# Performance work log

Measured on AMD Instinct MI355X. Metric: run time of the kernel, lower is better.

## Reference

```python
import jax, jax.numpy as jnp
import numpy as np

GAMMA = 1.0

def setup_inputs() -> dict:
    key = jax.random.key(0)
    kx, ky = jax.random.split(key)
    x = jax.random.normal(kx, (8192, 64), dtype=jnp.float32)
    y = jax.random.normal(ky, (8192, 64), dtype=jnp.float32)
    return {"x": x, "y": y}

def reference(x, y):
    # RBF kernel K[b,a] = exp(-gamma * ||x_b - y_a||^2)
    # broadcast intermediate of the naive formulation (same math).
    x_sq = jnp.sum(x * x, axis=-1)                    # (B,)
    y_sq = jnp.sum(y * y, axis=-1)                    # (A,)
    xy = jnp.einsum('bd,ad->ba', x, y)                # (B, A) GEMM
    dist_sq = x_sq[:, None] + y_sq[None, :] - 2.0 * xy
    dist_sq = jnp.maximum(dist_sq, 0.0)               # numeric floor
    return jnp.exp(-GAMMA * dist_sq)
```

## Files before the change

kernel.cpp:

```cpp
#include <hip/hip_runtime.h>

#define D    64
#define NROW 8192

typedef _Float16 f16x8 __attribute__((ext_vector_type(8)));
typedef float    f32x4 __attribute__((ext_vector_type(4)));

__global__ __launch_bounds__(256, 3) void rbf_fused(const float* __restrict__ x,
                                                    const float* __restrict__ y,
                                                    float* __restrict__ out) {
    __shared__ __align__(16) char YH[16384];
    __shared__ __align__(16) char YL[16384];
    __shared__ float Ysq0[128];
    __shared__ float Ysq1[128];

    const int t    = threadIdx.x;
    const int col0 = blockIdx.x * 128;
    const int row0 = blockIdx.y * 128;

    {
        const int r    = t & 127;
        const int half = t >> 7;
        const int swz  = (r & 7) << 4;
        const float* yp = y + (size_t)(col0 + r) * D + half * 32;
        float ssq = 0.f;
#pragma unroll
        for (int it = 0; it < 4; ++it) {
            float4 b0 = *reinterpret_cast<const float4*>(yp + it * 8);
            float4 b1 = *reinterpret_cast<const float4*>(yp + it * 8 + 4);
            float v[8] = {b0.x, b0.y, b0.z, b0.w, b1.x, b1.y, b1.z, b1.w};
            f16x8 h, l;
#pragma unroll
            for (int j = 0; j < 8; ++j) {
                _Float16 hh = (_Float16)v[j];
                h[j] = hh;
                l[j] = (_Float16)(v[j] - (float)hh);
                ssq  = fmaf(v[j], v[j], ssq);
            }
            const int off = r * 128 + ((half * 64 + it * 16) ^ swz);
            *reinterpret_cast<f16x8*>(YH + off) = h;
            *reinterpret_cast<f16x8*>(YL + off) = l;
        }
        if (half == 0) Ysq0[r] = ssq; else Ysq1[r] = ssq;
    }

    const int lane = t & 63;
    const int w    = t >> 6;
    const int l15  = lane & 15;
    const int lg   = lane >> 4;

    f16x8 xh[2][2], xl[2][2];
    float xsq[2];
#pragma unroll
    for (int i = 0; i < 2; ++i) {
        const float* xp = x + (size_t)(row0 + w * 32 + i * 16 + l15) * D + lg * 8;
        float s = 0.f;
#pragma unroll
        for (int kh = 0; kh < 2; ++kh) {
            float4 a0 = *reinterpret_cast<const float4*>(xp + kh * 32);
            float4 a1 = *reinterpret_cast<const float4*>(xp + kh * 32 + 4);
            float v[8] = {a0.x, a0.y, a0.z, a0.w, a1.x, a1.y, a1.z, a1.w};
#pragma unroll
            for (int j = 0; j < 8; ++j) {
                _Float16 hh = (_Float16)v[j];
                xh[i][kh][j] = hh;
                xl[i][kh][j] = (_Float16)(v[j] - (float)hh);
                s = fmaf(v[j], v[j], s);
            }
        }
        s += __shfl_xor(s, 16);
        s += __shfl_xor(s, 32);
        xsq[i] = s;
    }
    __syncthreads();

    f32x4 acc[2][8];
#pragma unroll
    for (int i = 0; i < 2; ++i)
#pragma unroll
        for (int nt = 0; nt < 8; ++nt) acc[i][nt] = (f32x4){0.f, 0.f, 0.f, 0.f};

    const int swzA = (l15 & 7) << 4;
#pragma unroll
    for (int kh = 0; kh < 2; ++kh) {
        const int dsw = (kh * 64 + lg * 16) ^ swzA;
#pragma unroll
        for (int nt = 0; nt < 8; ++nt) {
            const int aoff = (nt * 16 + l15) * 128 + dsw;
            f16x8 yh = *reinterpret_cast<const f16x8*>(YH + aoff);
            f16x8 yl = *reinterpret_cast<const f16x8*>(YL + aoff);
            acc[0][nt] = __builtin_amdgcn_mfma_f32_16x16x32_f16(yh, xh[0][kh], acc[0][nt], 0, 0, 0);
            acc[1][nt] = __builtin_amdgcn_mfma_f32_16x16x32_f16(yh, xh[1][kh], acc[1][nt], 0, 0, 0);
            acc[0][nt] = __builtin_amdgcn_mfma_f32_16x16x32_f16(yl, xh[0][kh], acc[0][nt], 0, 0, 0);
            acc[1][nt] = __builtin_amdgcn_mfma_f32_16x16x32_f16(yl, xh[1][kh], acc[1][nt], 0, 0, 0);
            acc[0][nt] = __builtin_amdgcn_mfma_f32_16x16x32_f16(yh, xl[0][kh], acc[0][nt], 0, 0, 0);
            acc[1][nt] = __builtin_amdgcn_mfma_f32_16x16x32_f16(yh, xl[1][kh], acc[1][nt], 0, 0, 0);
        }
    }

#pragma unroll
    for (int nt = 0; nt < 8; ++nt) {
        const int c = nt * 16 + lg * 4;
        float4 p0 = *reinterpret_cast<const float4*>(&Ysq0[c]);
        float4 p1 = *reinterpret_cast<const float4*>(&Ysq1[c]);
        float ysqv[4] = {p0.x + p1.x, p0.y + p1.y, p0.z + p1.z, p0.w + p1.w};
#pragma unroll
        for (int i = 0; i < 2; ++i) {
            const int rowg = row0 + w * 32 + i * 16 + l15;
            float e[4];
#pragma unroll
            for (int r = 0; r < 4; ++r) {
                float d2 = fmaf(-2.f, acc[i][nt][r], xsq[i] + ysqv[r]);
                d2 = fmaxf(d2, 0.f);
                e[r] = __expf(-d2);
            }
            *reinterpret_cast<float4*>(out + (size_t)rowg * NROW + col0 + c) =
                make_float4(e[0], e[1], e[2], e[3]);
        }
    }
}

extern "C" void kernel_launch(void* const* d_in, const int* in_sizes, int n_in,
                              void* d_out, int out_size, void* d_ws, size_t ws_size,
                              hipStream_t stream) {
    const float* x = (const float*)d_in[0];
    const float* y = (const float*)d_in[1];
    float* out = (float*)d_out;
    (void)d_ws; (void)ws_size;

    rbf_fused<<<dim3(NROW / 128, NROW / 128), 256, 0, stream>>>(x, y, out);
}
```

Measured before the change: 67.22 us.

## Precompute fp16 hi/lo splits and row norms in a prepass kernel

Adds a prepass kernel that converts x and y once into fp16 hi/lo planes plus squared norms in the workspace. The main kernel then loads these directly, so the per-block float-to-half splitting and norm reductions, which were repeated by every block in a row or column of the grid, go away. In exchange it adds an extra kernel launch and workspace traffic, and it falls back to the fused kernel when the workspace is too small. The main kernel is output-write bound (256MB), so the gain may be small.

Result: slower. 72.79 us (+8.3%).

```diff
diff --git a/kernel.cpp b/kernel.cpp
--- a/kernel.cpp
+++ b/kernel.cpp
@@ -5,6 +5,128 @@
 
 typedef _Float16 f16x8 __attribute__((ext_vector_type(8)));
 typedef float    f32x4 __attribute__((ext_vector_type(4)));
+
+__global__ __launch_bounds__(256) void rbf_split(const float* __restrict__ x,
+                                                 const float* __restrict__ y,
+                                                 _Float16* __restrict__ hi,
+                                                 _Float16* __restrict__ lo,
+                                                 float* __restrict__ sq) {
+    const int tid    = blockIdx.x * 256 + threadIdx.x;
+    const int rowAll = tid >> 3;
+    const int dp     = (tid & 7) * 8;
+    const float* src = (rowAll < NROW) ? (x + (size_t)rowAll * D)
+                                       : (y + (size_t)(rowAll - NROW) * D);
+    float4 a0 = *reinterpret_cast<const float4*>(src + dp);
+    float4 a1 = *reinterpret_cast<const float4*>(src + dp + 4);
+    float v[8] = {a0.x, a0.y, a0.z, a0.w, a1.x, a1.y, a1.z, a1.w};
+    f16x8 h, l;
+    float s = 0.f;
+#pragma unroll
+    for (int j = 0; j < 8; ++j) {
+        _Float16 hh = (_Float16)v[j];
+        h[j] = hh;
+        l[j] = (_Float16)(v[j] - (float)hh);
+        s = fmaf(v[j], v[j], s);
+    }
+    *reinterpret_cast<f16x8*>(hi + (size_t)rowAll * D + dp) = h;
+    *reinterpret_cast<f16x8*>(lo + (size_t)rowAll * D + dp) = l;
+    s += __shfl_xor(s, 1);
+    s += __shfl_xor(s, 2);
+    s += __shfl_xor(s, 4);
+    if ((tid & 7) == 0) sq[rowAll] = s;
+}
+
+__global__ __launch_bounds__(256, 3) void rbf_main2(const _Float16* __restrict__ hi,
+                                                    const _Float16* __restrict__ lo,
+                                                    const float* __restrict__ sq,
+                                                    float* __restrict__ out) {
+    __shared__ __align__(16) char YH[16384];
+    __shared__ __align__(16) char YL[16384];
+
+    const int t    = threadIdx.x;
+    const int col0 = blockIdx.x * 128;
+    const int row0 = blockIdx.y * 128;
+
+    {
+        const int r   = t & 127;
+        const int hb  = t >> 7;
+        const int swz = (r & 7) << 4;
+        const _Float16* gh = hi + (size_t)(NROW + col0 + r) * D;
+        const _Float16* gl = lo + (size_t)(NROW + col0 + r) * D;
+#pragma unroll
+        for (int it = 0; it < 4; ++it) {
+            const int c16 = hb * 4 + it;
+            const int off = r * 128 + ((c16 * 16) ^ swz);
+            *reinterpret_cast<f16x8*>(YH + off) =
+                *reinterpret_cast<const f16x8*>(gh + c16 * 8);
+            *reinterpret_cast<f16x8*>(YL + off) =
+                *reinterpret_cast<const f16x8*>(gl + c16 * 8);
+        }
+    }
+
+    const int lane = t & 63;
+    const int w    = t >> 6;
+    const int l15  = lane & 15;
+    const int lg   = lane >> 4;
+
+    f16x8 xh[2][2], xl[2][2];
+    float xsq[2];
+#pragma unroll
+    for (int i = 0; i < 2; ++i) {
+        const size_t xoff = (size_t)(row0 + w * 32 + i * 16 + l15) * D + lg * 8;
+#pragma unroll
+        for (int kh = 0; kh < 2; ++kh) {
+            xh[i][kh] = *reinterpret_cast<const f16x8*>(hi + xoff + kh * 32);
+            xl[i][kh] = *reinterpret_cast<const f16x8*>(lo + xoff + kh * 32);
+        }
+        xsq[i] = sq[row0 + w * 32 + i * 16 + l15];
+    }
+    __syncthreads();
+
+    f32x4 acc[2][8];
+#pragma unroll
+    for (int i = 0; i < 2; ++i)
+#pragma unroll
+        for (int nt = 0; nt < 8; ++nt) acc[i][nt] = (f32x4){0.f, 0.f, 0.f, 0.f};
+
+    const int swzA = (l15 & 7) << 4;
+#pragma unroll
+    for (int kh = 0; kh < 2; ++kh) {
+        const int dsw = (kh * 64 + lg * 16) ^ swzA;
+#pragma unroll
+        for (int nt = 0; nt < 8; ++nt) {
+            const int aoff = (nt * 16 + l15) * 128 + dsw;
+            f16x8 ah = *reinterpret_cast<const f16x8*>(YH + aoff);
+            f16x8 al = *reinterpret_cast<const f16x8*>(YL + aoff);
+            acc[0][nt] = __builtin_amdgcn_mfma_f32_16x16x32_f16(ah, xh[0][kh], acc[0][nt], 0, 0, 0);
+            acc[1][nt] = __builtin_amdgcn_mfma_f32_16x16x32_f16(ah, xh[1][kh], acc[1][nt], 0, 0, 0);
+            acc[0][nt] = __builtin_amdgcn_mfma_f32_16x16x32_f16(al, xh[0][kh], acc[0][nt], 0, 0, 0);
+            acc[1][nt] = __builtin_amdgcn_mfma_f32_16x16x32_f16(al, xh[1][kh], acc[1][nt], 0, 0, 0);
+            acc[0][nt] = __builtin_amdgcn_mfma_f32_16x16x32_f16(ah, xl[0][kh], acc[0][nt], 0, 0, 0);
+            acc[1][nt] = __builtin_amdgcn_mfma_f32_16x16x32_f16(ah, xl[1][kh], acc[1][nt], 0, 0, 0);
+        }
+    }
+
+#pragma unroll
+    for (int nt = 0; nt < 8; ++nt) {
+        const int c = nt * 16 + lg * 4;
+        float4 q = *reinterpret_cast<const float4*>(sq + NROW + col0 + c);
+        float ysqv[4] = {q.x, q.y, q.z, q.w};
+#pragma unroll
+        for (int i = 0; i < 2; ++i) {
+            const int rowg = row0 + w * 32 + i * 16 + l15;
+            float e[4];
+#pragma unroll
+            for (int r = 0; r < 4; ++r) {
+                float d2 = fmaf(-2.f, acc[i][nt][r], xsq[i] + ysqv[r]);
+                d2 = fmaxf(d2, 0.f);
+                e[r] = __expf(-d2);
+            }
+            *reinterpret_cast<float4*>(out + (size_t)rowg * NROW + col0 + c) =
+                make_float4(e[0], e[1], e[2], e[3]);
+        }
+    }
+}
 
 __global__ __launch_bounds__(256, 3) void rbf_fused(const float* __restrict__ x,
                                                     const float* __restrict__ y,
@@ -126,7 +248,17 @@
     const float* x = (const float*)d_in[0];
     const float* y = (const float*)d_in[1];
     float* out = (float*)d_out;
-    (void)d_ws; (void)ws_size;
-
-    rbf_fused<<<dim3(NROW / 128, NROW / 128), 256, 0, stream>>>(x, y, out);
-}
+
+    const size_t planeElems = (size_t)2 * NROW * D;
+    const size_t need = planeElems * sizeof(_Float16) * 2
+                      + (size_t)2 * NROW * sizeof(float);
+    if (ws_size >= need) {
+        _Float16* hi = (_Float16*)d_ws;
+        _Float16* lo = hi + planeElems;
+        float* sq    = (float*)(lo + planeElems);
+        rbf_split<<<512, 256, 0, stream>>>(x, y, hi, lo, sq);
+        rbf_main2<<<dim3(NROW / 128, NROW / 128), 256, 0, stream>>>(hi, lo, sq, out);
+    } else {
+        rbf_fused<<<dim3(NROW / 128, NROW / 128), 256, 0, stream>>>(x, y, out);
+    }
+}
```

## Persist Y tile across eight row tiles with double-buffered X prefetch

Applied to the files above, without the earlier changes.

Replaces the 4096-block grid with 512 blocks. Each block converts one 128-column Y tile into shared memory once, then loops over eight 128-row X tiles. The X loads for the next tile are issued before the current tile's MFMA and exp epilogue, so global latency is meant to overlap with compute, and the repeated Y staging and launch overhead go away. The trade-off is fewer blocks, which may leave CUs underused with 256 CUs and 2 blocks per CU, and higher register pressure from the prefetch buffers.

Result: slower. 92.22 us (+37.2%).

```diff
diff --git a/kernel.cpp b/kernel.cpp
--- a/kernel.cpp
+++ b/kernel.cpp
@@ -6,17 +6,18 @@
 typedef _Float16 f16x8 __attribute__((ext_vector_type(8)));
 typedef float    f32x4 __attribute__((ext_vector_type(4)));
 
-__global__ __launch_bounds__(256, 3) void rbf_fused(const float* __restrict__ x,
-                                                    const float* __restrict__ y,
-                                                    float* __restrict__ out) {
+__global__ __launch_bounds__(256, 2) void rbf_pipe(const float* __restrict__ x,
+                                                   const float* __restrict__ y,
+                                                   float* __restrict__ out) {
     __shared__ __align__(16) char YH[16384];
     __shared__ __align__(16) char YL[16384];
     __shared__ float Ysq0[128];
     __shared__ float Ysq1[128];
 
-    const int t    = threadIdx.x;
-    const int col0 = blockIdx.x * 128;
-    const int row0 = blockIdx.y * 128;
+    const int t       = threadIdx.x;
+    const int b       = blockIdx.x;
+    const int col0    = (b & 63) * 128;
+    const int rowbase = (b >> 6) * 1024;
 
     {
         const int r    = t & 127;
@@ -43,80 +44,102 @@
         }
         if (half == 0) Ysq0[r] = ssq; else Ysq1[r] = ssq;
     }
+    __syncthreads();
 
     const int lane = t & 63;
     const int w    = t >> 6;
     const int l15  = lane & 15;
     const int lg   = lane >> 4;
+    const int swzA = (l15 & 7) << 4;
 
-    f16x8 xh[2][2], xl[2][2];
-    float xsq[2];
+    float4 PA[2][2][2], PB[2][2][2];
+
+    auto LOADX = [&](int rt, float4 (&P)[2][2][2]) {
 #pragma unroll
-    for (int i = 0; i < 2; ++i) {
-        const float* xp = x + (size_t)(row0 + w * 32 + i * 16 + l15) * D + lg * 8;
-        float s = 0.f;
+        for (int i = 0; i < 2; ++i) {
+            const float* xp = x + (size_t)(rowbase + rt * 128 + w * 32 + i * 16 + l15) * D + lg * 8;
+            P[i][0][0] = *reinterpret_cast<const float4*>(xp);
+            P[i][0][1] = *reinterpret_cast<const float4*>(xp + 4);
+            P[i][1][0] = *reinterpret_cast<const float4*>(xp + 32);
+            P[i][1][1] = *reinterpret_cast<const float4*>(xp + 36);
+        }
+    };
+
+    auto TILE = [&](const float4 (&P)[2][2][2], int rt) {
+        f16x8 xh[2][2], xl[2][2];
+        float xsq[2];
+#pragma unroll
+        for (int i = 0; i < 2; ++i) {
+            float s = 0.f;
+#pragma unroll
+            for (int kh = 0; kh < 2; ++kh) {
+                float v[8] = {P[i][kh][0].x, P[i][kh][0].y, P[i][kh][0].z, P[i][kh][0].w,
+                              P[i][kh][1].x, P[i][kh][1].y, P[i][kh][1].z, P[i][kh][1].w};
+#pragma unroll
+                for (int j = 0; j < 8; ++j) {
+                    _Float16 hh = (_Float16)v[j];
+                    xh[i][kh][j] = hh;
+                    xl[i][kh][j] = (_Float16)(v[j] - (float)hh);
+                    s = fmaf(v[j], v[j], s);
+                }
+            }
+            s += __shfl_xor(s, 16);
+            s += __shfl_xor(s, 32);
+            xsq[i] = s;
+        }
+
+        f32x4 acc[2][8];
+#pragma unroll
+        for (int i = 0; i < 2; ++i)
+#pragma unroll
+            for (int nt = 0; nt < 8; ++nt) acc[i][nt] = (f32x4){0.f, 0.f, 0.f, 0.f};
+
 #pragma unroll
         for (int kh = 0; kh < 2; ++kh) {
-            float4 a0 = *reinterpret_cast<const float4*>(xp + kh * 32);
-            float4 a1 = *reinterpret_cast<const float4*>(xp + kh * 32 + 4);
-            float v[8] = {a0.x, a0.y, a0.z, a0.w, a1.x, a1.y, a1.z, a1.w};
+            const int dsw = (kh * 64 + lg * 16) ^ swzA;
 #pragma unroll
-            for (int j = 0; j < 8; ++j) {
-                _Float16 hh = (_Float16)v[j];
-                xh[i][kh][j] = hh;
-                xl[i][kh][j] = (_Float16)(v[j] - (float)hh);
-                s = fmaf(v[j], v[j], s);
+            for (int nt = 0; nt < 8; ++nt) {
+                const int aoff = (nt * 16 + l15) * 128 + dsw;
+                f16x8 yh = *reinterpret_cast<const f16x8*>(YH + aoff);
+                f16x8 yl = *reinterpret_cast<const f16x8*>(YL + aoff);
+                acc[0][nt] = __builtin_amdgcn_mfma_f32_16x16x32_f16(yh, xh[0][kh], acc[0][nt], 0, 0, 0);
+                acc[1][nt] = __builtin_amdgcn_mfma_f32_16x16x32_f16(yh, xh[1][kh], acc[1][nt], 0, 0, 0);
+                acc[0][nt] = __builtin_amdgcn_mfma_f32_16x16x32_f16(yl, xh[0][kh], acc[0][nt], 0, 0, 0);
+                acc[1][nt] = __builtin_amdgcn_mfma_f32_16x16x32_f16(yl, xh[1][kh], acc[1][nt], 0, 0, 0);
+                acc[0][nt] = __builtin_amdgcn_mfma_f32_16x16x32_f16(yh, xl[0][kh], acc[0][nt], 0, 0, 0);
+                acc[1][nt] = __builtin_amdgcn_mfma_f32_16x16x32_f16(yh, xl[1][kh], acc[1][nt], 0, 0, 0);
             }
         }
-        s += __shfl_xor(s, 16);
-        s += __shfl_xor(s, 32);
-        xsq[i] = s;
-    }
-    __syncthreads();
 
-    f32x4 acc[2][8];
-#pragma unroll
-    for (int i = 0; i < 2; ++i)
-#pragma unroll
-        for (int nt = 0; nt < 8; ++nt) acc[i][nt] = (f32x4){0.f, 0.f, 0.f, 0.f};
-
-    const int swzA = (l15 & 7) << 4;
-#pragma unroll
-    for (int kh = 0; kh < 2; ++kh) {
-        const int dsw = (kh * 64 + lg * 16) ^ swzA;
 #pragma unroll
         for (int nt = 0; nt < 8; ++nt) {
-            const int aoff = (nt * 16 + l15) * 128 + dsw;
-            f16x8 yh = *reinterpret_cast<const f16x8*>(YH + aoff);
-            f16x8 yl = *reinterpret_cast<const f16x8*>(YL + aoff);
-            acc[0][nt] = __builtin_amdgcn_mfma_f32_16x16x32_f16(yh, xh[0][kh], acc[0][nt], 0, 0, 0);
-            acc[1][nt] = __builtin_amdgcn_mfma_f32_16x16x32_f16(yh, xh[1][kh], acc[1][nt], 0, 0, 0);
-            acc[0][nt] = __builtin_amdgcn_mfma_f32_16x16x32_f16(yl, xh[0][kh], acc[0][nt], 0, 0, 0);
-            acc[1][nt] = __builtin_amdgcn_mfma_f32_16x16x32_f16(yl, xh[1][kh], acc[1][nt], 0, 0, 0);
-            acc[0][nt] = __builtin_amdgcn_mfma_f32_16x16x32_f16(yh, xl[0][kh], acc[0][nt], 0, 0, 0);
-            acc[1][nt] = __builtin_amdgcn_mfma_f32_16x16x32_f16(yh, xl[1][kh], acc[1][nt], 0, 0, 0);
+            const int c = nt * 16 + lg * 4;
+            float4 p0 = *reinterpret_cast<const float4*>(&Ysq0[c]);
+            float4 p1 = *reinterpret_cast<const float4*>(&Ysq1[c]);
+            float ysqv[4] = {p0.x + p1.x, p0.y + p1.y, p0.z + p1.z, p0.w + p1.w};
+#pragma unroll
+            for (int i = 0; i < 2; ++i) {
+                const int rowg = rowbase + rt * 128 + w * 32 + i * 16 + l15;
+                float e[4];
+#pragma unroll
+                for (int r = 0; r < 4; ++r) {
+                    float d2 = fmaf(-2.f, acc[i][nt][r], xsq[i] + ysqv[r]);
+                    d2 = fmaxf(d2, 0.f);
+                    e[r] = __expf(-d2);
+                }
+                *reinterpret_cast<float4*>(out + (size_t)rowg * NROW + col0 + c) =
+                    make_float4(e[0], e[1], e[2], e[3]);
+            }
         }
-    }
+    };
 
+    LOADX(0, PA);
 #pragma unroll
-    for (int nt = 0; nt < 8; ++nt) {
-        const int c = nt * 16 + lg * 4;
-        float4 p0 = *reinterpret_cast<const float4*>(&Ysq0[c]);
-        float4 p1 = *reinterpret_cast<const float4*>(&Ysq1[c]);
-        float ysqv[4] = {p0.x + p1.x, p0.y + p1.y, p0.z + p1.z, p0.w + p1.w};
-#pragma unroll
-        for (int i = 0; i < 2; ++i) {
-            const int rowg = row0 + w * 32 + i * 16 + l15;
-            float e[4];
-#pragma unroll
-            for (int r = 0; r < 4; ++r) {
-                float d2 = fmaf(-2.f, acc[i][nt][r], xsq[i] + ysqv[r]);
-                d2 = fmaxf(d2, 0.f);
-                e[r] = __expf(-d2);
-            }
-            *reinterpret_cast<float4*>(out + (size_t)rowg * NROW + col0 + c) =
-                make_float4(e[0], e[1], e[2], e[3]);
-        }
+    for (int tp = 0; tp < 4; ++tp) {
+        LOADX(2 * tp + 1, PB);
+        TILE(PA, 2 * tp);
+        if (tp < 3) LOADX(2 * tp + 2, PA);
+        TILE(PB, 2 * tp + 1);
     }
 }
 
@@ -128,5 +151,5 @@
     float* out = (float*)d_out;
     (void)d_ws; (void)ws_size;
 
-    rbf_fused<<<dim3(NROW / 128, NROW / 128), 256, 0, stream>>>(x, y, out);
+    rbf_pipe<<<dim3(512), 256, 0, stream>>>(x, y, out);
 }
```
